# Kernel optimization log

Measured on AMD Instinct MI355X. Metric: run time of the kernel, lower is better.

Reference implementation:

```python
import jax, jax.numpy as jnp
import numpy as np

N_AUTHOR, N_FOS, N_INST, N_PAPER = 100000, 30000, 8000, 200000
D_IN, D_OUT = 128, 128
# (name, n_src, n_dst, n_edges)
RELS = [("aff", N_AUTHOR, N_INST, 150000), ("ita", N_INST, N_AUTHOR, 150000),
        ("writes", N_AUTHOR, N_PAPER, 500000), ("pta", N_PAPER, N_AUTHOR, 500000),
        ("cites", N_PAPER, N_PAPER, 1000000), ("topic", N_PAPER, N_FOS, 500000),
        ("ftp", N_FOS, N_PAPER, 500000)]
NODE_SIZES = {"author": N_AUTHOR, "fos": N_FOS, "inst": N_INST, "paper": N_PAPER}


def setup_inputs() -> dict:
    key = jax.random.key(0)
    ks = iter(jax.random.split(key, 64))
    inp = {}
    for nt, n in NODE_SIZES.items():
        inp[f"x_{nt}"] = jax.random.normal(next(ks), (n, D_IN), jnp.float32)
    for name, ns, nd, e in RELS:
        inp[f"src_{name}"] = jax.random.randint(next(ks), (e,), 0, ns, jnp.int64)
        inp[f"dst_{name}"] = jax.random.randint(next(ks), (e,), 0, nd, jnp.int64)
    w_scale = 1.0 / np.sqrt(D_IN)
    for nt in NODE_SIZES:
        inp[f"W_root_{nt}"] = jax.random.uniform(next(ks), (D_IN, D_OUT), jnp.float32, -w_scale, w_scale)
        inp[f"b_root_{nt}"] = jax.random.uniform(next(ks), (D_OUT,), jnp.float32, -w_scale, w_scale)
    for name, _, _, _ in RELS:
        inp[f"W_{name}"] = jax.random.uniform(next(ks), (D_IN, D_OUT), jnp.float32, -w_scale, w_scale)
    return inp


def _mean_agg(x_src, src, dst, n_dst):
    # gather source features along edges, mean-reduce into destinations
    msg = x_src[src]                                             # [E, D_IN]
    s = jax.ops.segment_sum(msg, dst, num_segments=n_dst)        # [n_dst, D_IN]
    cnt = jax.ops.segment_sum(jnp.ones_like(dst, dtype=x_src.dtype), dst, num_segments=n_dst)
    return s / jnp.maximum(cnt, 1.0)[:, None]                    # isolated nodes -> 0


def reference(x_author, x_fos, x_inst, x_paper,
              W_root_author, b_root_author, W_root_fos, b_root_fos,
              W_root_inst, b_root_inst, W_root_paper, b_root_paper,
              W_aff, W_ita, W_writes, W_pta, W_cites, W_topic, W_ftp,
              src_aff, dst_aff, src_ita, dst_ita, src_writes, dst_writes,
              src_pta, dst_pta, src_cites, dst_cites, src_topic, dst_topic,
              src_ftp, dst_ftp):
    # root (self) transforms
    out_author = x_author @ W_root_author + b_root_author
    out_fos = x_fos @ W_root_fos + b_root_fos
    out_inst = x_inst @ W_root_inst + b_root_inst
    out_paper = x_paper @ W_root_paper + b_root_paper
    # per-relation aggregate -> linear -> accumulate into destination type
    out_inst = out_inst + _mean_agg(x_author, src_aff, dst_aff, N_INST) @ W_aff
    out_author = out_author + _mean_agg(x_inst, src_ita, dst_ita, N_AUTHOR) @ W_ita
    out_paper = out_paper + _mean_agg(x_author, src_writes, dst_writes, N_PAPER) @ W_writes
    out_author = out_author + _mean_agg(x_paper, src_pta, dst_pta, N_AUTHOR) @ W_pta
    out_paper = out_paper + _mean_agg(x_paper, src_cites, dst_cites, N_PAPER) @ W_cites
    out_fos = out_fos + _mean_agg(x_paper, src_topic, dst_topic, N_FOS) @ W_topic
    out_paper = out_paper + _mean_agg(x_fos, src_ftp, dst_ftp, N_PAPER) @ W_ftp
    # concatenate per-type outputs (author, fos, inst, paper) along node axis
    return jnp.concatenate([out_author, out_fos, out_inst, out_paper], axis=0)
```

## Files before the change

### kernel.cpp

```cpp
#include <hip/hip_runtime.h>

#define N_AUTHOR 100000
#define N_FOS    30000
#define N_INST   8000
#define N_PAPER  200000

typedef __attribute__((ext_vector_type(8))) short short8v;
typedef __attribute__((ext_vector_type(4))) float float4v;

__device__ __forceinline__ unsigned short f2bf(float f) {
  unsigned u = __float_as_uint(f);
  u = u + 0x7fffu + ((u >> 16) & 1u);
  return (unsigned short)(u >> 16);
}

#define O_CNT    0
#define O_OFFS   3352000
#define O_CURSOR 6704000
#define O_BTOT   10056000
#define O_CSR    10060096
#define O_WT     23260096
#define NCNT     838000

struct RelTab { const int* src; const int* dst; int E; int base; };
struct Rels { RelTab r[7]; };
struct WPtrs { const float* w[11]; };

__global__ void conv_w(WPtrs P, unsigned short* __restrict__ wt) {
  int idx = blockIdx.x * 256 + threadIdx.x;
  if (idx >= 11 * 16384) return;
  int mat = idx >> 14, rem = idx & 16383;
  int k = rem >> 7, n = rem & 127;
  float v = P.w[mat][rem];
  wt[mat * 16384 + n * 128 + k] = f2bf(v);
}

__global__ void count_k(Rels R, int* __restrict__ cnt) {
  int gsz = gridDim.x * blockDim.x;
  int gtid = blockIdx.x * blockDim.x + threadIdx.x;
  for (int rr = 0; rr < 7; ++rr) {
    const int* dst = R.r[rr].dst;
    int E = R.r[rr].E, base = R.r[rr].base;
    for (int e = gtid; e < E; e += gsz) atomicAdd(&cnt[base + dst[e]], 1);
  }
}

__global__ void scan1(const int* __restrict__ cnt, int* __restrict__ offs,
                      int* __restrict__ btot, int n) {
  __shared__ int sh[256];
  int tid = threadIdx.x;
  int base = blockIdx.x * 2048 + tid * 8;
  int v[8]; int s = 0;
  #pragma unroll
  for (int i = 0; i < 8; ++i) { v[i] = (base + i < n) ? cnt[base + i] : 0; s += v[i]; }
  sh[tid] = s; __syncthreads();
  for (int off = 1; off < 256; off <<= 1) {
    int t = (tid >= off) ? sh[tid - off] : 0;
    __syncthreads();
    sh[tid] += t;
    __syncthreads();
  }
  int excl = sh[tid] - s;
  if (tid == 255) btot[blockIdx.x] = sh[255];
  int run = excl;
  #pragma unroll
  for (int i = 0; i < 8; ++i) { if (base + i < n) offs[base + i] = run; run += v[i]; }
}

__global__ void scan2(int* __restrict__ btot, int nb) {
  __shared__ int sh[512];
  int tid = threadIdx.x;
  int v = (tid < nb) ? btot[tid] : 0;
  sh[tid] = v; __syncthreads();
  for (int off = 1; off < 512; off <<= 1) {
    int t = (tid >= off) ? sh[tid - off] : 0;
    __syncthreads();
    sh[tid] += t;
    __syncthreads();
  }
  if (tid < nb) btot[tid] = sh[tid] - v;
}

__global__ void scan3(int* __restrict__ offs, int* __restrict__ cursor,
                      const int* __restrict__ btot, int n) {
  int gsz = gridDim.x * blockDim.x;
  for (int idx = blockIdx.x * blockDim.x + threadIdx.x; idx < n; idx += gsz) {
    int b = idx >> 11;
    int v = offs[idx] + btot[b];
    offs[idx] = v;
    cursor[idx] = v;
  }
}

__global__ void fill_k(Rels R, int* __restrict__ cursor, int* __restrict__ csr) {
  int gsz = gridDim.x * blockDim.x;
  int gtid = blockIdx.x * blockDim.x + threadIdx.x;
  for (int rr = 0; rr < 7; ++rr) {
    const int* src = R.r[rr].src;
    const int* dst = R.r[rr].dst;
    int E = R.r[rr].E, base = R.r[rr].base;
    for (int e = gtid; e < E; e += gsz) {
      int p = atomicAdd(&cursor[base + dst[e]], 1);
      csr[p] = src[e];
    }
  }
}

struct GemmSrc { const float* x; const unsigned short* wt; int cntBase; };
struct TypeArgs {
  GemmSrc s[4];
  int nsrc;
  int bstart;
  int n;
  const float* bias;
  float* out;
};
struct AllArgs {
  TypeArgs t[4];
  const int* offs;
  const int* cnt;
  const int* csr;
};

__global__ __launch_bounds__(256, 4) void rgcn_gemm(AllArgs A) {
  __shared__ unsigned short a_lds[64 * 128];
  const int tid = threadIdx.x;
  const int wv = tid >> 6, lane = tid & 63;
  const int q = lane >> 4;
  const int c0 = (lane & 15) * 8;

  int bid = blockIdx.x;
  int ty = (bid >= A.t[3].bstart) ? 3 : (bid >= A.t[2].bstart) ? 2
         : (bid >= A.t[1].bstart) ? 1 : 0;
  const TypeArgs& T = A.t[ty];
  const int rb = (bid - T.bstart) * 64;
  const int n = T.n;

  float4v acc[8];
  #pragma unroll
  for (int i = 0; i < 8; ++i) acc[i] = (float4v)0.0f;

  for (int kb = 0; kb < T.nsrc; ++kb) {
    const GemmSrc S = T.s[kb];
    if (S.cntBase < 0) {
      #pragma unroll
      for (int i = 0; i < 4; ++i) {
        int c = tid + i * 256;
        int r = c >> 4, cc = (c & 15) * 8;
        int g = rb + r;
        short8v hv;
        if (g < n) {
          float4 v0 = *(const float4*)(S.x + (size_t)g * 128 + cc);
          float4 v1 = *(const float4*)(S.x + (size_t)g * 128 + cc + 4);
          hv[0] = (short)f2bf(v0.x); hv[1] = (short)f2bf(v0.y);
          hv[2] = (short)f2bf(v0.z); hv[3] = (short)f2bf(v0.w);
          hv[4] = (short)f2bf(v1.x); hv[5] = (short)f2bf(v1.y);
          hv[6] = (short)f2bf(v1.z); hv[7] = (short)f2bf(v1.w);
        } else {
          hv = (short8v)0;
        }
        int byte = r * 256 + cc * 2; byte ^= (r & 7) << 4;
        *(short8v*)((char*)a_lds + byte) = hv;
      }
    } else {
      int stA[4], dgA[4];
      #pragma unroll
      for (int rd = 0; rd < 4; ++rd) {
        int r = wv * 16 + rd * 4 + q;
        int g = rb + r;
        int gc = (g < n) ? g : (n - 1);
        int gd = S.cntBase + gc;
        stA[rd] = A.offs[gd];
        dgA[rd] = (g < n) ? A.cnt[gd] : 0;
      }
      #pragma unroll
      for (int rd = 0; rd < 4; ++rd) {
        int r = wv * 16 + rd * 4 + q;
        int st = stA[rd], deg = dgA[rd];
        float a0 = 0.f, a1 = 0.f, a2 = 0.f, a3 = 0.f;
        float a4 = 0.f, a5 = 0.f, a6 = 0.f, a7 = 0.f;
        int j = 0;
        for (; j + 2 <= deg; j += 2) {
          int s0 = A.csr[st + j], s1 = A.csr[st + j + 1];
          const float* p0 = S.x + (size_t)s0 * 128 + c0;
          const float* p1 = S.x + (size_t)s1 * 128 + c0;
          float4 u0 = *(const float4*)p0;
          float4 u1 = *(const float4*)(p0 + 4);
          float4 v0 = *(const float4*)p1;
          float4 v1 = *(const float4*)(p1 + 4);
          a0 += u0.x + v0.x; a1 += u0.y + v0.y;
          a2 += u0.z + v0.z; a3 += u0.w + v0.w;
          a4 += u1.x + v1.x; a5 += u1.y + v1.y;
          a6 += u1.z + v1.z; a7 += u1.w + v1.w;
        }
        if (j < deg) {
          int s0 = A.csr[st + j];
          const float* p0 = S.x + (size_t)s0 * 128 + c0;
          float4 u0 = *(const float4*)p0;
          float4 u1 = *(const float4*)(p0 + 4);
          a0 += u0.x; a1 += u0.y; a2 += u0.z; a3 += u0.w;
          a4 += u1.x; a5 += u1.y; a6 += u1.z; a7 += u1.w;
        }
        float sc = 1.0f / (float)((deg > 0) ? deg : 1);
        short8v hv;
        hv[0] = (short)f2bf(a0 * sc); hv[1] = (short)f2bf(a1 * sc);
        hv[2] = (short)f2bf(a2 * sc); hv[3] = (short)f2bf(a3 * sc);
        hv[4] = (short)f2bf(a4 * sc); hv[5] = (short)f2bf(a5 * sc);
        hv[6] = (short)f2bf(a6 * sc); hv[7] = (short)f2bf(a7 * sc);
        int byte = r * 256 + c0 * 2; byte ^= (r & 7) << 4;
        *(short8v*)((char*)a_lds + byte) = hv;
      }
    }
    __syncthreads();
    short8v af[4];
    #pragma unroll
    for (int ks = 0; ks < 4; ++ks) {
      int r = wv * 16 + (lane & 15);
      int ch = ks * 4 + (lane >> 4);
      int byte = r * 256 + ch * 16; byte ^= (r & 7) << 4;
      af[ks] = *(const short8v*)((const char*)a_lds + byte);
    }
    const unsigned short* wbase = S.wt + (size_t)(lane & 15) * 128
                                + (size_t)(lane >> 4) * 8;
    #pragma unroll
    for (int ct = 0; ct < 8; ++ct) {
      short8v bfr[4];
      #pragma unroll
      for (int ks = 0; ks < 4; ++ks)
        bfr[ks] = *(const short8v*)(wbase + (size_t)ct * 16 * 128 + ks * 32);
      #pragma unroll
      for (int ks = 0; ks < 4; ++ks)
        acc[ct] = __builtin_amdgcn_mfma_f32_16x16x32_bf16(af[ks], bfr[ks], acc[ct], 0, 0, 0);
    }
    __syncthreads();
  }
  #pragma unroll
  for (int ct = 0; ct < 8; ++ct) {
    #pragma unroll
    for (int i = 0; i < 4; ++i) {
      int row = wv * 16 + (lane >> 4) * 4 + i;
      int g = rb + row;
      if (g < n) {
        int col = ct * 16 + (lane & 15);
        T.out[(size_t)g * 128 + col] = acc[ct][i] + T.bias[col];
      }
    }
  }
}

extern "C" void kernel_launch(void* const* d_in, const int* in_sizes, int n_in,
                              void* d_out, int out_size, void* d_ws, size_t ws_size,
                              hipStream_t stream) {
  const float* x_author = (const float*)d_in[0];
  const float* x_fos    = (const float*)d_in[1];
  const float* x_inst   = (const float*)d_in[2];
  const float* x_paper  = (const float*)d_in[3];

  Rels R;
  const int E[7]  = {150000, 150000, 500000, 500000, 1000000, 500000, 500000};
  const int ND[7] = {N_INST, N_AUTHOR, N_PAPER, N_AUTHOR, N_PAPER, N_FOS, N_PAPER};
  int base = 0;
  for (int r = 0; r < 7; ++r) {
    R.r[r].src = (const int*)d_in[4 + 2 * r];
    R.r[r].dst = (const int*)d_in[5 + 2 * r];
    R.r[r].E = E[r];
    R.r[r].base = base;
    base += ND[r];
  }

  char* ws = (char*)d_ws;
  int* cnt    = (int*)(ws + O_CNT);
  int* offs   = (int*)(ws + O_OFFS);
  int* cursor = (int*)(ws + O_CURSOR);
  int* btot   = (int*)(ws + O_BTOT);
  int* csr    = (int*)(ws + O_CSR);
  unsigned short* wt = (unsigned short*)(ws + O_WT);

  WPtrs WP;
  WP.w[0] = (const float*)d_in[18];
  WP.w[1] = (const float*)d_in[20];
  WP.w[2] = (const float*)d_in[22];
  WP.w[3] = (const float*)d_in[24];
  for (int r = 0; r < 7; ++r) WP.w[4 + r] = (const float*)d_in[26 + r];

  conv_w<<<704, 256, 0, stream>>>(WP, wt);
  hipMemsetAsync(cnt, 0, (size_t)NCNT * 4, stream);
  count_k<<<1024, 256, 0, stream>>>(R, cnt);
  scan1<<<410, 256, 0, stream>>>(cnt, offs, btot, NCNT);
  scan2<<<1, 512, 0, stream>>>(btot, 410);
  scan3<<<1024, 256, 0, stream>>>(offs, cursor, btot, NCNT);
  fill_k<<<1024, 256, 0, stream>>>(R, cursor, csr);

  float* out = (float*)d_out;
  const int B_AFF = 0, B_ITA = 8000, B_WRITES = 108000, B_PTA = 308000,
            B_CITES = 408000, B_TOPIC = 608000, B_FTP = 638000;

  AllArgs A;
  A.offs = offs; A.cnt = cnt; A.csr = csr;
  for (int t = 0; t < 4; ++t)
    for (int i = 0; i < 4; ++i) A.t[t].s[i] = GemmSrc{nullptr, nullptr, 0};

  const int NB_AUTHOR = (N_AUTHOR + 63) / 64;
  const int NB_FOS    = (N_FOS + 63) / 64;
  const int NB_INST   = (N_INST + 63) / 64;
  const int NB_PAPER  = (N_PAPER + 63) / 64;

  A.t[0].s[0] = GemmSrc{x_author, wt + 0 * 16384, -1};
  A.t[0].s[1] = GemmSrc{x_inst,   wt + 5 * 16384, B_ITA};
  A.t[0].s[2] = GemmSrc{x_paper,  wt + 7 * 16384, B_PTA};
  A.t[0].nsrc = 3; A.t[0].bstart = 0; A.t[0].n = N_AUTHOR;
  A.t[0].bias = (const float*)d_in[19]; A.t[0].out = out;
  A.t[1].s[0] = GemmSrc{x_fos,   wt + 1 * 16384, -1};
  A.t[1].s[1] = GemmSrc{x_paper, wt + 9 * 16384, B_TOPIC};
  A.t[1].nsrc = 2; A.t[1].bstart = NB_AUTHOR; A.t[1].n = N_FOS;
  A.t[1].bias = (const float*)d_in[21]; A.t[1].out = out + (size_t)100000 * 128;
  A.t[2].s[0] = GemmSrc{x_inst,   wt + 2 * 16384, -1};
  A.t[2].s[1] = GemmSrc{x_author, wt + 4 * 16384, B_AFF};
  A.t[2].nsrc = 2; A.t[2].bstart = NB_AUTHOR + NB_FOS; A.t[2].n = N_INST;
  A.t[2].bias = (const float*)d_in[23]; A.t[2].out = out + (size_t)130000 * 128;
  A.t[3].s[0] = GemmSrc{x_paper,  wt + 3 * 16384, -1};
  A.t[3].s[1] = GemmSrc{x_author, wt + 6 * 16384, B_WRITES};
  A.t[3].s[2] = GemmSrc{x_paper,  wt + 8 * 16384, B_CITES};
  A.t[3].s[3] = GemmSrc{x_fos,    wt + 10 * 16384, B_FTP};
  A.t[3].nsrc = 4; A.t[3].bstart = NB_AUTHOR + NB_FOS + NB_INST; A.t[3].n = N_PAPER;
  A.t[3].bias = (const float*)d_in[25]; A.t[3].out = out + (size_t)138000 * 128;

  const int NB_TOTAL = NB_AUTHOR + NB_FOS + NB_INST + NB_PAPER;
  rgcn_gemm<<<NB_TOTAL, 256, 0, stream>>>(A);
}
```

Baseline: 917.2 us.

## Pre-convert node features to bf16 and gather bf16 rows in aggregation

Adds a prep kernel that converts all node feature matrices to bf16 copies in the workspace, along with weight conversion and count zeroing, replacing a memset. The fused gather-mean-GEMM kernel then gathers bf16 rows with one row per 4 threads, halving bytes per edge. It also merges the two final scan kernels into one. This needs a larger workspace and adds a full conversion pass. Rounding inputs before summation slightly changes numerics.

```diff
diff --git a/kernel.cpp b/kernel.cpp
--- a/kernel.cpp
+++ b/kernel.cpp
@@ -12,6 +12,12 @@
   unsigned u = __float_as_uint(f);
   u = u + 0x7fffu + ((u >> 16) & 1u);
   return (unsigned short)(u >> 16);
+}
+#define BF2F(s) __uint_as_float(((unsigned)(unsigned short)(s)) << 16)
+
+__device__ __forceinline__ void acc8(float4v& x, float4v& y, short8v h) {
+  x[0] += BF2F(h[0]); x[1] += BF2F(h[1]); x[2] += BF2F(h[2]); x[3] += BF2F(h[3]);
+  y[0] += BF2F(h[4]); y[1] += BF2F(h[5]); y[2] += BF2F(h[6]); y[3] += BF2F(h[7]);
 }
 
 #define O_CNT    0
@@ -20,19 +26,48 @@
 #define O_BTOT   10056000
 #define O_CSR    10060096
 #define O_WT     23260096
+#define XB_AUTHOR 23620544
+#define XB_FOS    49220544
+#define XB_INST   56900544
+#define XB_PAPER  58948544
+#define WS_NEED_BF 110148544ULL
 #define NCNT     838000
 
 struct RelTab { const int* src; const int* dst; int E; int base; };
 struct Rels { RelTab r[7]; };
 struct WPtrs { const float* w[11]; };
-
-__global__ void conv_w(WPtrs P, unsigned short* __restrict__ wt) {
-  int idx = blockIdx.x * 256 + threadIdx.x;
-  if (idx >= 11 * 16384) return;
-  int mat = idx >> 14, rem = idx & 16383;
-  int k = rem >> 7, n = rem & 127;
-  float v = P.w[mat][rem];
-  wt[mat * 16384 + n * 128 + k] = f2bf(v);
+struct XCvt { const float* x; unsigned short* xb; int n8; };
+
+__global__ void prep(WPtrs P, unsigned short* __restrict__ wt,
+                     int* __restrict__ cnt, XCvt x0, XCvt x1, XCvt x2, XCvt x3,
+                     int doX) {
+  int gsz = gridDim.x * blockDim.x;
+  int gtid = blockIdx.x * blockDim.x + threadIdx.x;
+  for (int i = gtid; i < 11 * 16384; i += gsz) {
+    int mat = i >> 14, rem = i & 16383;
+    int k = rem >> 7, n = rem & 127;
+    wt[mat * 16384 + n * 128 + k] = f2bf(P.w[mat][rem]);
+  }
+  for (int i = gtid; i < NCNT; i += gsz) cnt[i] = 0;
+  if (doX) {
+    XCvt xc[4] = {x0, x1, x2, x3};
+    #pragma unroll
+    for (int a = 0; a < 4; ++a) {
+      const float* xp = xc[a].x;
+      short8v* xbp = (short8v*)xc[a].xb;
+      int n8 = xc[a].n8;
+      for (int i = gtid; i < n8; i += gsz) {
+        float4v v0 = *(const float4v*)(xp + (size_t)i * 8);
+        float4v v1 = *(const float4v*)(xp + (size_t)i * 8 + 4);
+        short8v h;
+        h[0] = (short)f2bf(v0[0]); h[1] = (short)f2bf(v0[1]);
+        h[2] = (short)f2bf(v0[2]); h[3] = (short)f2bf(v0[3]);
+        h[4] = (short)f2bf(v1[0]); h[5] = (short)f2bf(v1[1]);
+        h[6] = (short)f2bf(v1[2]); h[7] = (short)f2bf(v1[3]);
+        xbp[i] = h;
+      }
+    }
+  }
 }
 
 __global__ void count_k(Rels R, int* __restrict__ cnt) {
@@ -67,7 +102,8 @@
   for (int i = 0; i < 8; ++i) { if (base + i < n) offs[base + i] = run; run += v[i]; }
 }
 
-__global__ void scan2(int* __restrict__ btot, int nb) {
+__global__ void scan23(int* __restrict__ offs, int* __restrict__ cursor,
+                       const int* __restrict__ btot, int nb, int n) {
   __shared__ int sh[512];
   int tid = threadIdx.x;
   int v = (tid < nb) ? btot[tid] : 0;
@@ -78,17 +114,15 @@
     sh[tid] += t;
     __syncthreads();
   }
-  if (tid < nb) btot[tid] = sh[tid] - v;
-}
-
-__global__ void scan3(int* __restrict__ offs, int* __restrict__ cursor,
-                      const int* __restrict__ btot, int n) {
-  int gsz = gridDim.x * blockDim.x;
-  for (int idx = blockIdx.x * blockDim.x + threadIdx.x; idx < n; idx += gsz) {
-    int b = idx >> 11;
-    int v = offs[idx] + btot[b];
-    offs[idx] = v;
-    cursor[idx] = v;
+  int excl = sh[tid] - v;
+  __syncthreads();
+  sh[tid] = excl;
+  __syncthreads();
+  int gsz = gridDim.x * 512;
+  for (int idx = blockIdx.x * 512 + tid; idx < n; idx += gsz) {
+    int val = offs[idx] + sh[idx >> 11];
+    offs[idx] = val;
+    cursor[idx] = val;
   }
 }
 
@@ -106,7 +140,8 @@
   }
 }
 
-struct GemmSrc { const float* x; const unsigned short* wt; int cntBase; };
+struct GemmSrc { const float* x; const unsigned short* xb;
+                 const unsigned short* wt; int cntBase; };
 struct TypeArgs {
   GemmSrc s[4];
   int nsrc;
@@ -122,12 +157,13 @@
   const int* csr;
 };
 
+#define LD4(p) (*(const float4v*)(p))
+
+template <int BF>
 __global__ __launch_bounds__(256, 4) void rgcn_gemm(AllArgs A) {
   __shared__ unsigned short a_lds[64 * 128];
   const int tid = threadIdx.x;
   const int wv = tid >> 6, lane = tid & 63;
-  const int q = lane >> 4;
-  const int c0 = (lane & 15) * 8;
 
   int bid = blockIdx.x;
   int ty = (bid >= A.t[3].bstart) ? 3 : (bid >= A.t[2].bstart) ? 2
@@ -143,32 +179,96 @@
   for (int kb = 0; kb < T.nsrc; ++kb) {
     const GemmSrc S = T.s[kb];
     if (S.cntBase < 0) {
-      #pragma unroll
-      for (int i = 0; i < 4; ++i) {
-        int c = tid + i * 256;
-        int r = c >> 4, cc = (c & 15) * 8;
+      if (BF) {
+        int r = tid >> 2, cb = (tid & 3) * 64;
         int g = rb + r;
-        short8v hv;
-        if (g < n) {
-          float4 v0 = *(const float4*)(S.x + (size_t)g * 128 + cc);
-          float4 v1 = *(const float4*)(S.x + (size_t)g * 128 + cc + 4);
-          hv[0] = (short)f2bf(v0.x); hv[1] = (short)f2bf(v0.y);
-          hv[2] = (short)f2bf(v0.z); hv[3] = (short)f2bf(v0.w);
-          hv[4] = (short)f2bf(v1.x); hv[5] = (short)f2bf(v1.y);
-          hv[6] = (short)f2bf(v1.z); hv[7] = (short)f2bf(v1.w);
-        } else {
-          hv = (short8v)0;
+        const short8v* p = (const short8v*)(S.xb + (size_t)g * 128 + (cb >> 1));
+        #pragma unroll
+        for (int k = 0; k < 4; ++k) {
+          short8v h = (g < n) ? p[k] : (short8v)0;
+          int byte = (r * 256 + cb + k * 16) ^ ((r & 7) << 4);
+          *(short8v*)((char*)a_lds + byte) = h;
         }
-        int byte = r * 256 + cc * 2; byte ^= (r & 7) << 4;
-        *(short8v*)((char*)a_lds + byte) = hv;
-      }
+      } else {
+        #pragma unroll
+        for (int i = 0; i < 4; ++i) {
+          int c = tid + i * 256;
+          int r = c >> 4, cc = (c & 15) * 8;
+          int g = rb + r;
+          short8v hv;
+          if (g < n) {
+            float4v v0 = LD4(S.x + (size_t)g * 128 + cc);
+            float4v v1 = LD4(S.x + (size_t)g * 128 + cc + 4);
+            hv[0] = (short)f2bf(v0[0]); hv[1] = (short)f2bf(v0[1]);
+            hv[2] = (short)f2bf(v0[2]); hv[3] = (short)f2bf(v0[3]);
+            hv[4] = (short)f2bf(v1[0]); hv[5] = (short)f2bf(v1[1]);
+            hv[6] = (short)f2bf(v1[2]); hv[7] = (short)f2bf(v1[3]);
+          } else hv = (short8v)0;
+          int byte = r * 256 + cc * 2; byte ^= (r & 7) << 4;
+          *(short8v*)((char*)a_lds + byte) = hv;
+        }
+      }
+    } else if (BF) {
+      const int r = tid >> 2;
+      const int c0 = (tid & 3) * 32;
+      int g = rb + r;
+      int gd = S.cntBase + ((g < n) ? g : 0);
+      int st = A.offs[gd];
+      int deg = (g < n) ? A.cnt[gd] : 0;
+      float4v a0 = (float4v)0.f, a1 = (float4v)0.f, a2 = (float4v)0.f,
+              a3 = (float4v)0.f, a4 = (float4v)0.f, a5 = (float4v)0.f,
+              a6 = (float4v)0.f, a7 = (float4v)0.f;
+      int j = 0;
+      for (; j + 2 <= deg; j += 2) {
+        int i0 = A.csr[st + j], i1 = A.csr[st + j + 1];
+        const short8v* p0 = (const short8v*)(S.xb + (size_t)i0 * 128 + c0);
+        const short8v* p1 = (const short8v*)(S.xb + (size_t)i1 * 128 + c0);
+        short8v h0 = p0[0], h1 = p0[1], h2 = p0[2], h3 = p0[3];
+        short8v k0 = p1[0], k1 = p1[1], k2 = p1[2], k3 = p1[3];
+        acc8(a0, a1, h0); acc8(a2, a3, h1); acc8(a4, a5, h2); acc8(a6, a7, h3);
+        acc8(a0, a1, k0); acc8(a2, a3, k1); acc8(a4, a5, k2); acc8(a6, a7, k3);
+      }
+      if (j < deg) {
+        int i0 = A.csr[st + j];
+        const short8v* p0 = (const short8v*)(S.xb + (size_t)i0 * 128 + c0);
+        short8v h0 = p0[0], h1 = p0[1], h2 = p0[2], h3 = p0[3];
+        acc8(a0, a1, h0); acc8(a2, a3, h1); acc8(a4, a5, h2); acc8(a6, a7, h3);
+      }
+      float sc = 1.0f / (float)((deg > 0) ? deg : 1);
+      a0 *= sc; a1 *= sc; a2 *= sc; a3 *= sc;
+      a4 *= sc; a5 *= sc; a6 *= sc; a7 *= sc;
+      short8v o0, o1, o2, o3;
+      o0[0] = (short)f2bf(a0[0]); o0[1] = (short)f2bf(a0[1]);
+      o0[2] = (short)f2bf(a0[2]); o0[3] = (short)f2bf(a0[3]);
+      o0[4] = (short)f2bf(a1[0]); o0[5] = (short)f2bf(a1[1]);
+      o0[6] = (short)f2bf(a1[2]); o0[7] = (short)f2bf(a1[3]);
+      o1[0] = (short)f2bf(a2[0]); o1[1] = (short)f2bf(a2[1]);
+      o1[2] = (short)f2bf(a2[2]); o1[3] = (short)f2bf(a2[3]);
+      o1[4] = (short)f2bf(a3[0]); o1[5] = (short)f2bf(a3[1]);
+      o1[6] = (short)f2bf(a3[2]); o1[7] = (short)f2bf(a3[3]);
+      o2[0] = (short)f2bf(a4[0]); o2[1] = (short)f2bf(a4[1]);
+      o2[2] = (short)f2bf(a4[2]); o2[3] = (short)f2bf(a4[3]);
+      o2[4] = (short)f2bf(a5[0]); o2[5] = (short)f2bf(a5[1]);
+      o2[6] = (short)f2bf(a5[2]); o2[7] = (short)f2bf(a5[3]);
+      o3[0] = (short)f2bf(a6[0]); o3[1] = (short)f2bf(a6[1]);
+      o3[2] = (short)f2bf(a6[2]); o3[3] = (short)f2bf(a6[3]);
+      o3[4] = (short)f2bf(a7[0]); o3[5] = (short)f2bf(a7[1]);
+      o3[6] = (short)f2bf(a7[2]); o3[7] = (short)f2bf(a7[3]);
+      int bbase = r * 256 + c0 * 2;
+      int sw = (r & 7) << 4;
+      *(short8v*)((char*)a_lds + ((bbase) ^ sw)) = o0;
+      *(short8v*)((char*)a_lds + ((bbase + 16) ^ sw)) = o1;
+      *(short8v*)((char*)a_lds + ((bbase + 32) ^ sw)) = o2;
+      *(short8v*)((char*)a_lds + ((bbase + 48) ^ sw)) = o3;
     } else {
+      const int q = lane >> 4;
+      const int c0 = (lane & 15) * 8;
       int stA[4], dgA[4];
       #pragma unroll
       for (int rd = 0; rd < 4; ++rd) {
         int r = wv * 16 + rd * 4 + q;
         int g = rb + r;
-        int gc = (g < n) ? g : (n - 1);
+        int gc = (g < n) ? g : 0;
         int gd = S.cntBase + gc;
         stA[rd] = A.offs[gd];
         dgA[rd] = (g < n) ? A.cnt[gd] : 0;
@@ -184,22 +284,19 @@
           int s0 = A.csr[st + j], s1 = A.csr[st + j + 1];
           const float* p0 = S.x + (size_t)s0 * 128 + c0;
           const float* p1 = S.x + (size_t)s1 * 128 + c0;
-          float4 u0 = *(const float4*)p0;
-          float4 u1 = *(const float4*)(p0 + 4);
-          float4 v0 = *(const float4*)p1;
-          float4 v1 = *(const float4*)(p1 + 4);
-          a0 += u0.x + v0.x; a1 += u0.y + v0.y;
-          a2 += u0.z + v0.z; a3 += u0.w + v0.w;
-          a4 += u1.x + v1.x; a5 += u1.y + v1.y;
-          a6 += u1.z + v1.z; a7 += u1.w + v1.w;
+          float4v u0 = LD4(p0), u1 = LD4(p0 + 4);
+          float4v v0 = LD4(p1), v1 = LD4(p1 + 4);
+          a0 += u0[0] + v0[0]; a1 += u0[1] + v0[1];
+          a2 += u0[2] + v0[2]; a3 += u0[3] + v0[3];
+          a4 += u1[0] + v1[0]; a5 += u1[1] + v1[1];
+          a6 += u1[2] + v1[2]; a7 += u1[3] + v1[3];
         }
         if (j < deg) {
           int s0 = A.csr[st + j];
           const float* p0 = S.x + (size_t)s0 * 128 + c0;
-          float4 u0 = *(const float4*)p0;
-          float4 u1 = *(const float4*)(p0 + 4);
-          a0 += u0.x; a1 += u0.y; a2 += u0.z; a3 += u0.w;
-          a4 += u1.x; a5 += u1.y; a6 += u1.z; a7 += u1.w;
+          float4v u0 = LD4(p0), u1 = LD4(p0 + 4);
+          a0 += u0[0]; a1 += u0[1]; a2 += u0[2]; a3 += u0[3];
+          a4 += u1[0]; a5 += u1[1]; a6 += u1[2]; a7 += u1[3];
         }
         float sc = 1.0f / (float)((deg > 0) ? deg : 1);
         short8v hv;
@@ -275,6 +372,12 @@
   int* btot   = (int*)(ws + O_BTOT);
   int* csr    = (int*)(ws + O_CSR);
   unsigned short* wt = (unsigned short*)(ws + O_WT);
+  unsigned short* xbA = (unsigned short*)(ws + XB_AUTHOR);
+  unsigned short* xbF = (unsigned short*)(ws + XB_FOS);
+  unsigned short* xbI = (unsigned short*)(ws + XB_INST);
+  unsigned short* xbP = (unsigned short*)(ws + XB_PAPER);
+
+  const int useBF = (ws_size >= WS_NEED_BF) ? 1 : 0;
 
   WPtrs WP;
   WP.w[0] = (const float*)d_in[18];
@@ -283,12 +386,15 @@
   WP.w[3] = (const float*)d_in[24];
   for (int r = 0; r < 7; ++r) WP.w[4 + r] = (const float*)d_in[26 + r];
 
-  conv_w<<<704, 256, 0, stream>>>(WP, wt);
-  hipMemsetAsync(cnt, 0, (size_t)NCNT * 4, stream);
+  XCvt xcA = {x_author, xbA, N_AUTHOR * 16};
+  XCvt xcF = {x_fos,    xbF, N_FOS * 16};
+  XCvt xcI = {x_inst,   xbI, N_INST * 16};
+  XCvt xcP = {x_paper,  xbP, N_PAPER * 16};
+
+  prep<<<2048, 256, 0, stream>>>(WP, wt, cnt, xcA, xcF, xcI, xcP, useBF);
   count_k<<<1024, 256, 0, stream>>>(R, cnt);
   scan1<<<410, 256, 0, stream>>>(cnt, offs, btot, NCNT);
-  scan2<<<1, 512, 0, stream>>>(btot, 410);
-  scan3<<<1024, 256, 0, stream>>>(offs, cursor, btot, NCNT);
+  scan23<<<1024, 512, 0, stream>>>(offs, cursor, btot, 410, NCNT);
   fill_k<<<1024, 256, 0, stream>>>(R, cursor, csr);
 
   float* out = (float*)d_out;
@@ -298,33 +404,39 @@
   AllArgs A;
   A.offs = offs; A.cnt = cnt; A.csr = csr;
   for (int t = 0; t < 4; ++t)
-    for (int i = 0; i < 4; ++i) A.t[t].s[i] = GemmSrc{nullptr, nullptr, 0};
+    for (int i = 0; i < 4; ++i) A.t[t].s[i] = GemmSrc{nullptr, nullptr, nullptr, 0};
 
   const int NB_AUTHOR = (N_AUTHOR + 63) / 64;
   const int NB_FOS    = (N_FOS + 63) / 64;
   const int NB_INST   = (N_INST + 63) / 64;
   const int NB_PAPER  = (N_PAPER + 63) / 64;
 
-  A.t[0].s[0] = GemmSrc{x_author, wt + 0 * 16384, -1};
-  A.t[0].s[1] = GemmSrc{x_inst,   wt + 5 * 16384, B_ITA};
-  A.t[0].s[2] = GemmSrc{x_paper,  wt + 7 * 16384, B_PTA};
+  A.t[0].s[0] = GemmSrc{x_author, xbA, wt + 0 * 16384, -1};
+  A.t[0].s[1] = GemmSrc{x_inst,   xbI, wt + 5 * 16384, B_ITA};
+  A.t[0].s[2] = GemmSrc{x_paper,  xbP, wt + 7 * 16384, B_PTA};
   A.t[0].nsrc = 3; A.t[0].bstart = 0; A.t[0].n = N_AUTHOR;
   A.t[0].bias = (const float*)d_in[19]; A.t[0].out = out;
-  A.t[1].s[0] = GemmSrc{x_fos,   wt + 1 * 16384, -1};
-  A.t[1].s[1] = GemmSrc{x_paper, wt + 9 * 16384, B_TOPIC};
+
+  A.t[1].s[0] = GemmSrc{x_fos,   xbF, wt + 1 * 16384, -1};
+  A.t[1].s[1] = GemmSrc{x_paper, xbP, wt + 9 * 16384, B_TOPIC};
   A.t[1].nsrc = 2; A.t[1].bstart = NB_AUTHOR; A.t[1].n = N_FOS;
   A.t[1].bias = (const float*)d_in[21]; A.t[1].out = out + (size_t)100000 * 128;
-  A.t[2].s[0] = GemmSrc{x_inst,   wt + 2 * 16384, -1};
-  A.t[2].s[1] = GemmSrc{x_author, wt + 4 * 16384, B_AFF};
+
+  A.t[2].s[0] = GemmSrc{x_inst,   xbI, wt + 2 * 16384, -1};
+  A.t[2].s[1] = GemmSrc{x_author, xbA, wt + 4 * 16384, B_AFF};
   A.t[2].nsrc = 2; A.t[2].bstart = NB_AUTHOR + NB_FOS; A.t[2].n = N_INST;
   A.t[2].bias = (const float*)d_in[23]; A.t[2].out = out + (size_t)130000 * 128;
-  A.t[3].s[0] = GemmSrc{x_paper,  wt + 3 * 16384, -1};
-  A.t[3].s[1] = GemmSrc{x_author, wt + 6 * 16384, B_WRITES};
-  A.t[3].s[2] = GemmSrc{x_paper,  wt + 8 * 16384, B_CITES};
-  A.t[3].s[3] = GemmSrc{x_fos,    wt + 10 * 16384, B_FTP};
+
+  A.t[3].s[0] = GemmSrc{x_paper,  xbP, wt + 3 * 16384, -1};
+  A.t[3].s[1] = GemmSrc{x_author, xbA, wt + 6 * 16384, B_WRITES};
+  A.t[3].s[2] = GemmSrc{x_paper,  xbP, wt + 8 * 16384, B_CITES};
+  A.t[3].s[3] = GemmSrc{x_fos,    xbF, wt + 10 * 16384, B_FTP};
   A.t[3].nsrc = 4; A.t[3].bstart = NB_AUTHOR + NB_FOS + NB_INST; A.t[3].n = N_PAPER;
   A.t[3].bias = (const float*)d_in[25]; A.t[3].out = out + (size_t)138000 * 128;
 
   const int NB_TOTAL = NB_AUTHOR + NB_FOS + NB_INST + NB_PAPER;
-  rgcn_gemm<<<NB_TOTAL, 256, 0, stream>>>(A);
-}
+  if (useBF)
+    rgcn_gemm<1><<<NB_TOTAL, 256, 0, stream>>>(A);
+  else
+    rgcn_gemm<0><<<NB_TOTAL, 256, 0, stream>>>(A);
+}
```

New measurement: 900.3 us. Within noise of the previous version (-1.8%).
